# Kernel optimization log

Hardware: AMD Instinct MI355X
Metric: run time of the kernel (lower is better)

Reference implementation:

```python
import jax, jax.numpy as jnp
import numpy as np

B, S, D = 16, 4096, 64
SCALE = float(np.sqrt(D))  # sqrt(hidden_size)


def setup_inputs() -> dict:
    key = jax.random.key(0)
    kq, kk, kv = jax.random.split(key, 3)
    return {
        "query": jax.random.normal(kq, (B, S, D), dtype=jnp.float32),
        "key": jax.random.normal(kk, (B, S, D), dtype=jnp.float32),
        "value": jax.random.normal(kv, (B, S, D), dtype=jnp.float32),
    }


def reference(query, key, value):
    # energy: [B, S, S]
    energy = jnp.einsum("bqd,bkd->bqk", query, key) / SCALE
    attention = jax.nn.softmax(energy, axis=2)
    return jnp.einsum("bqk,bkd->bqd", attention, value)
```

## Files before the change

### kernel.cpp

```cpp
#include <hip/hip_runtime.h>


#define NBATCH 16
#define SEQ    4096
#define DIM    64
#define BQ     128
#define BK     64
#define NKT    (SEQ / BK)
#define NTILES (NBATCH * NKT)
#define TILEH  4096

#define QSCALE 0.180336879f

typedef _Float16 half2_t __attribute__((ext_vector_type(2)));
typedef _Float16 half4_t __attribute__((ext_vector_type(4)));
typedef _Float16 half8_t __attribute__((ext_vector_type(8)));
typedef float    floatx4 __attribute__((ext_vector_type(4)));

__device__ inline float fast_exp2(float x) {
#if __has_builtin(__builtin_amdgcn_exp2f)
  return __builtin_amdgcn_exp2f(x);
#else
  return exp2f(x);
#endif
}
__device__ inline float fast_rcp(float x) {
#if __has_builtin(__builtin_amdgcn_rcpf)
  return __builtin_amdgcn_rcpf(x);
#else
  return 1.0f / x;
#endif
}

__device__ inline int swz(int row, int col) {
  return row * 64 + ((((col >> 3) ^ ((row >> 1) & 7)) << 3) | (col & 7));
}

__device__ inline void async16(const void* g, void* l) {
  __builtin_amdgcn_global_load_lds(
      (const __attribute__((address_space(1))) void*)g,
      (__attribute__((address_space(3))) void*)l, 16, 0, 0);
}

__global__ __launch_bounds__(256, 2)
void prepack_kv(const float* __restrict__ Kg, const float* __restrict__ Vg,
                _Float16* __restrict__ Kh, _Float16* __restrict__ Vh)
{
  __shared__ __align__(16) _Float16 sVi[TILEH];
  const int tid = threadIdx.x;
  const int t16 = tid & 15;
  const int kg  = tid >> 4;
  const int bt  = blockIdx.x;
  const float* Kt_ = Kg + (size_t)bt * BK * DIM;
  const float* Vt_ = Vg + (size_t)bt * BK * DIM;

  floatx4 kbuf[4], vbuf[4];
  #pragma unroll
  for (int i = 0; i < 4; ++i) {
    const int key = kg + 16 * i;
    kbuf[i] = *(const floatx4*)(Kt_ + key * DIM + t16 * 4);
    vbuf[i] = *(const floatx4*)(Vt_ + key * DIM + t16 * 4);
  }
  {
    const int vbase = (kg >> 2) * 8 + (kg & 3) * 2;
    #pragma unroll
    for (int e = 0; e < 4; ++e) {
      const int dim = t16 * 4 + e;
      half2_t h0; h0[0] = (_Float16)vbuf[0][e]; h0[1] = (_Float16)vbuf[1][e];
      half2_t h1; h1[0] = (_Float16)vbuf[2][e]; h1[1] = (_Float16)vbuf[3][e];
      *(half2_t*)&sVi[swz(dim, vbase)]      = h0;
      *(half2_t*)&sVi[swz(dim, vbase + 32)] = h1;
    }
  }
  {
    _Float16* Ko = Kh + (size_t)bt * TILEH;
    #pragma unroll
    for (int i = 0; i < 4; ++i) {
      const int key = kg + 16 * i;
      half4_t h;
      #pragma unroll
      for (int j = 0; j < 4; ++j) h[j] = (_Float16)kbuf[i][j];
      *(half4_t*)&Ko[swz(key, t16 * 4)] = h;
    }
  }
  __syncthreads();
  half8_t* Vo = (half8_t*)(Vh + (size_t)bt * TILEH);
  const half8_t* Vs = (const half8_t*)sVi;
  Vo[tid] = Vs[tid]; Vo[tid + 256] = Vs[tid + 256];
}

__global__ __launch_bounds__(256, 2)
void attn_f16_flash(const float* __restrict__ Qg, const _Float16* __restrict__ Kh,
                    const _Float16* __restrict__ Vh, float* __restrict__ Og)
{
  __shared__ __align__(16) _Float16 sT[4][2 * TILEH];

  const int tid  = threadIdx.x;
  const int wave = tid >> 6;
  const int lane = tid & 63;
  const int l16  = lane & 15;
  const int quad = lane >> 4;
  const int hK   = (l16 >> 1) & 7;

  const int bid  = blockIdx.x;
  const int x    = bid & 7;
  const int r    = bid >> 3;
  const int b    = x + ((r & 1) << 3);
  const int qt   = r >> 1;
  const int q0   = qt * BQ + wave * 32;

  const float* Qb = Qg + ((size_t)b * SEQ + q0) * DIM;
  float*       Ob = Og + ((size_t)b * SEQ + q0) * DIM;

  half8_t qf[2][2];
  #pragma unroll
  for (int s = 0; s < 2; ++s)
    #pragma unroll
    for (int c = 0; c < 2; ++c) {
      const floatx4 f0 = *(const floatx4*)(Qb + (s * 16 + l16) * DIM + c * 32 + quad * 8);
      const floatx4 f1 = *(const floatx4*)(Qb + (s * 16 + l16) * DIM + c * 32 + quad * 8 + 4);
      half8_t h;
      #pragma unroll
      for (int j = 0; j < 4; ++j) h[j] = (_Float16)(f0[j] * QSCALE);
      #pragma unroll
      for (int j = 0; j < 4; ++j) h[4 + j] = (_Float16)(f1[j] * QSCALE);
      qf[s][c] = h;
    }

  half8_t vones;
  #pragma unroll
  for (int j = 0; j < 8; ++j) vones[j] = (_Float16)1.0f;

  floatx4 oacc2[4][2];
  floatx4 lacc[2];
  #pragma unroll
  for (int n = 0; n < 4; ++n)
    #pragma unroll
    for (int s = 0; s < 2; ++s) oacc2[n][s] = (floatx4){0.f, 0.f, 0.f, 0.f};
  #pragma unroll
  for (int s = 0; s < 2; ++s) lacc[s] = (floatx4){0.f, 0.f, 0.f, 0.f};

  #define ASYNC(KT, BUF)                                                       \
    do {                                                                       \
      const char* gk = (const char*)(Kh + ((size_t)b * NKT + (KT)) * TILEH)    \
                       + wave * 2048;                                          \
      const char* gv = (const char*)(Vh + ((size_t)b * NKT + (KT)) * TILEH)    \
                       + wave * 2048;                                          \
      char* lk = (char*)(&sT[BUF][0])     + wave * 2048;                       \
      char* lv = (char*)(&sT[BUF][TILEH]) + wave * 2048;                       \
      async16(gk + lane * 16,        lk);                                      \
      async16(gk + 1024 + lane * 16, lk + 1024);                               \
      async16(gv + lane * 16,        lv);                                      \
      async16(gv + 1024 + lane * 16, lv + 1024);                               \
    } while (0)

  #define QKH(scX, BUF, H)                                                     \
    do {                                                                       \
      const _Float16* SKB = &sT[BUF][0];                                       \
      _Pragma("unroll")                                                        \
      for (int k2 = 0; k2 < 2; ++k2)                                           \
        _Pragma("unroll")                                                      \
        for (int s = 0; s < 2; ++s) scX[k2][s] = (floatx4){0.f, 0.f, 0.f, 0.f};\
      _Pragma("unroll")                                                        \
      for (int k2 = 0; k2 < 2; ++k2) {                                         \
        const int nk = (H) * 2 + k2;                                           \
        _Pragma("unroll")                                                      \
        for (int c = 0; c < 2; ++c) {                                          \
          half8_t kf = *(const half8_t*)&SKB[(nk * 16 + l16) * 64 +            \
                                             (((c * 4 + quad) ^ hK) << 3)];    \
          _Pragma("unroll")                                                    \
          for (int s = 0; s < 2; ++s)                                          \
            scX[k2][s] = __builtin_amdgcn_mfma_f32_16x16x32_f16(               \
                kf, qf[s][c], scX[k2][s], 0, 0, 0);                            \
        }                                                                      \
      }                                                                        \
    } while (0)

  #define EXPH(scX, bfrX)                                                      \
    do {                                                                       \
      _Pragma("unroll")                                                        \
      for (int s = 0; s < 2; ++s) {                                            \
        half8_t bf;                                                            \
        _Pragma("unroll")                                                      \
        for (int j = 0; j < 8; ++j)                                            \
          bf[j] = (_Float16)fast_exp2(scX[j & 1][s][j >> 1]);                  \
        bfrX[s] = bf;                                                          \
      }                                                                        \
    } while (0)

  #define PVH(bfrX, BUF, H)                                                    \
    do {                                                                       \
      const _Float16* SVB = &sT[BUF][TILEH];                                   \
      _Pragma("unroll")                                                        \
      for (int n = 0; n < 4; ++n) {                                            \
        half8_t vf = *(const half8_t*)&SVB[(n * 16 + l16) * 64 +               \
                                           ((((H) * 4 + quad) ^ hK) << 3)];    \
        _Pragma("unroll")                                                      \
        for (int s = 0; s < 2; ++s)                                            \
          oacc2[n][s] = __builtin_amdgcn_mfma_f32_16x16x32_f16(                \
              vf, bfrX[s], oacc2[n][s], 0, 0, 0);                              \
      }                                                                        \
      _Pragma("unroll")                                                        \
      for (int s = 0; s < 2; ++s)                                              \
        lacc[s] = __builtin_amdgcn_mfma_f32_16x16x32_f16(                      \
            vones, bfrX[s], lacc[s], 0, 0, 0);                                 \
    } while (0)

  #define GATE(N)                                                              \
    do {                                                                       \
      asm volatile("s_waitcnt vmcnt(" #N ")" ::: "memory");                    \
      __builtin_amdgcn_s_barrier();                                            \
      __builtin_amdgcn_sched_barrier(0);                                       \
    } while (0)

  floatx4 scA[2][2], scB[2][2];
  half8_t bfrA[2], bfrB[2];

  #define STEP(TT, CB)                                                         \
    do {                                                                       \
      QKH(scB, CB, 1);                                \
      EXPH(scA, bfrA);                           \
      PVH(bfrA, CB, 0);                       \
      GATE(4);                                                                 \
      ASYNC((TT) + 3, ((CB) + 3) & 3);                                         \
      QKH(scA, ((CB) + 1) & 3, 0);           \
      EXPH(scB, bfrB);                                                         \
      PVH(bfrB, CB, 1);                      \
    } while (0)

  ASYNC(0, 0);
  ASYNC(1, 1);
  GATE(4);
  ASYNC(2, 2);
  QKH(scA, 0, 0);

  #pragma unroll 1
  for (int t = 0; t < NKT - 4; t += 4) {
    STEP(t + 0, 0);
    STEP(t + 1, 1);
    STEP(t + 2, 2);
    STEP(t + 3, 3);
  }
  STEP(60, 0);

  QKH(scB, 1, 1);
  EXPH(scA, bfrA);
  PVH(bfrA, 1, 0);
  GATE(4);
  QKH(scA, 2, 0);
  EXPH(scB, bfrB);
  PVH(bfrB, 1, 1);

  {
    QKH(scB, 2, 1);
    EXPH(scA, bfrA);
    PVH(bfrA, 2, 0);
    GATE(0);
    QKH(scA, 3, 0);
    EXPH(scB, bfrB);
    PVH(bfrB, 2, 1);
  }
  {
    QKH(scB, 3, 1);
    EXPH(scA, bfrA);
    PVH(bfrA, 3, 0);
    EXPH(scB, bfrB);
    PVH(bfrB, 3, 1);
  }

  #pragma unroll
  for (int s = 0; s < 2; ++s) {
    const float inv = fast_rcp(lacc[s][0]);
    #pragma unroll
    for (int n = 0; n < 4; ++n) {
      floatx4 o = oacc2[n][s];
      #pragma unroll
      for (int j = 0; j < 4; ++j) o[j] *= inv;
      *(floatx4*)&Ob[(s * 16 + l16) * DIM + n * 16 + quad * 4] = o;
    }
  }

  #undef ASYNC
  #undef QKH
  #undef EXPH
  #undef PVH
  #undef GATE
  #undef STEP
}

extern "C" void kernel_launch(void* const* d_in, const int* in_sizes, int n_in,
                              void* d_out, int out_size, void* d_ws, size_t ws_size,
                              hipStream_t stream) {
  const float* Q = (const float*)d_in[0];
  const float* K = (const float*)d_in[1];
  const float* V = (const float*)d_in[2];
  float* O  = (float*)d_out;
  (void)in_sizes; (void)n_in; (void)out_size; (void)ws_size;

  _Float16* Kh = (_Float16*)d_ws;
  _Float16* Vh = Kh + (size_t)NTILES * TILEH;

  prepack_kv<<<dim3(NTILES), dim3(256), 0, stream>>>(K, V, Kh, Vh);
  attn_f16_flash<<<dim3(NBATCH * (SEQ / BQ)), dim3(256), 0, stream>>>(
      Q, Kh, Vh, O);
}
```

Before: 156.4 us.

## Split each query tile across eight waves with sixteen rows per wave

The block grows from 256 to 512 threads and each wave now handles 16 query rows instead of 32. The per-wave Q fragments, score, exp and accumulator arrays shrink to one sub-tile, and the async K/V tile copy is spread over eight waves with one 16-byte load per lane each. Wait counts drop to match. This cuts register pressure and adds waves for latency hiding, but halves how many MFMAs reuse each LDS K/V fragment, so LDS read traffic per FLOP doubles.

```diff
diff --git a/kernel.cpp b/kernel.cpp
--- a/kernel.cpp
+++ b/kernel.cpp
@@ -89,7 +89,7 @@
   Vo[tid] = Vs[tid]; Vo[tid + 256] = Vs[tid + 256];
 }
 
-__global__ __launch_bounds__(256, 2)
+__global__ __launch_bounds__(512, 4)
 void attn_f16_flash(const float* __restrict__ Qg, const _Float16* __restrict__ Kh,
                     const _Float16* __restrict__ Vh, float* __restrict__ Og)
 {
@@ -107,60 +107,51 @@
   const int r    = bid >> 3;
   const int b    = x + ((r & 1) << 3);
   const int qt   = r >> 1;
-  const int q0   = qt * BQ + wave * 32;
+  const int q0   = qt * BQ + wave * 16;
 
   const float* Qb = Qg + ((size_t)b * SEQ + q0) * DIM;
   float*       Ob = Og + ((size_t)b * SEQ + q0) * DIM;
 
-  half8_t qf[2][2];
-  #pragma unroll
-  for (int s = 0; s < 2; ++s)
-    #pragma unroll
-    for (int c = 0; c < 2; ++c) {
-      const floatx4 f0 = *(const floatx4*)(Qb + (s * 16 + l16) * DIM + c * 32 + quad * 8);
-      const floatx4 f1 = *(const floatx4*)(Qb + (s * 16 + l16) * DIM + c * 32 + quad * 8 + 4);
-      half8_t h;
-      #pragma unroll
-      for (int j = 0; j < 4; ++j) h[j] = (_Float16)(f0[j] * QSCALE);
-      #pragma unroll
-      for (int j = 0; j < 4; ++j) h[4 + j] = (_Float16)(f1[j] * QSCALE);
-      qf[s][c] = h;
-    }
+  half8_t qf[2];
+  #pragma unroll
+  for (int c = 0; c < 2; ++c) {
+    const floatx4 f0 = *(const floatx4*)(Qb + l16 * DIM + c * 32 + quad * 8);
+    const floatx4 f1 = *(const floatx4*)(Qb + l16 * DIM + c * 32 + quad * 8 + 4);
+    half8_t h;
+    #pragma unroll
+    for (int j = 0; j < 4; ++j) h[j] = (_Float16)(f0[j] * QSCALE);
+    #pragma unroll
+    for (int j = 0; j < 4; ++j) h[4 + j] = (_Float16)(f1[j] * QSCALE);
+    qf[c] = h;
+  }
 
   half8_t vones;
   #pragma unroll
   for (int j = 0; j < 8; ++j) vones[j] = (_Float16)1.0f;
 
-  floatx4 oacc2[4][2];
-  floatx4 lacc[2];
-  #pragma unroll
-  for (int n = 0; n < 4; ++n)
-    #pragma unroll
-    for (int s = 0; s < 2; ++s) oacc2[n][s] = (floatx4){0.f, 0.f, 0.f, 0.f};
-  #pragma unroll
-  for (int s = 0; s < 2; ++s) lacc[s] = (floatx4){0.f, 0.f, 0.f, 0.f};
+  floatx4 oacc[4];
+  floatx4 lacc;
+  #pragma unroll
+  for (int n = 0; n < 4; ++n) oacc[n] = (floatx4){0.f, 0.f, 0.f, 0.f};
+  lacc = (floatx4){0.f, 0.f, 0.f, 0.f};
 
   #define ASYNC(KT, BUF)                                                       \
     do {                                                                       \
       const char* gk = (const char*)(Kh + ((size_t)b * NKT + (KT)) * TILEH)    \
-                       + wave * 2048;                                          \
+                       + wave * 1024;                                          \
       const char* gv = (const char*)(Vh + ((size_t)b * NKT + (KT)) * TILEH)    \
-                       + wave * 2048;                                          \
-      char* lk = (char*)(&sT[BUF][0])     + wave * 2048;                       \
-      char* lv = (char*)(&sT[BUF][TILEH]) + wave * 2048;                       \
-      async16(gk + lane * 16,        lk);                                      \
-      async16(gk + 1024 + lane * 16, lk + 1024);                               \
-      async16(gv + lane * 16,        lv);                                      \
-      async16(gv + 1024 + lane * 16, lv + 1024);                               \
+                       + wave * 1024;                                          \
+      char* lk = (char*)(&sT[BUF][0])     + wave * 1024;                       \
+      char* lv = (char*)(&sT[BUF][TILEH]) + wave * 1024;                       \
+      async16(gk + lane * 16, lk);                                             \
+      async16(gv + lane * 16, lv);                                             \
     } while (0)
 
   #define QKH(scX, BUF, H)                                                     \
     do {                                                                       \
       const _Float16* SKB = &sT[BUF][0];                                       \
       _Pragma("unroll")                                                        \
-      for (int k2 = 0; k2 < 2; ++k2)                                           \
-        _Pragma("unroll")                                                      \
-        for (int s = 0; s < 2; ++s) scX[k2][s] = (floatx4){0.f, 0.f, 0.f, 0.f};\
+      for (int k2 = 0; k2 < 2; ++k2) scX[k2] = (floatx4){0.f, 0.f, 0.f, 0.f};  \
       _Pragma("unroll")                                                        \
       for (int k2 = 0; k2 < 2; ++k2) {                                         \
         const int nk = (H) * 2 + k2;                                           \
@@ -168,24 +159,19 @@
         for (int c = 0; c < 2; ++c) {                                          \
           half8_t kf = *(const half8_t*)&SKB[(nk * 16 + l16) * 64 +            \
                                              (((c * 4 + quad) ^ hK) << 3)];    \
-          _Pragma("unroll")                                                    \
-          for (int s = 0; s < 2; ++s)                                          \
-            scX[k2][s] = __builtin_amdgcn_mfma_f32_16x16x32_f16(               \
-                kf, qf[s][c], scX[k2][s], 0, 0, 0);                            \
+          scX[k2] = __builtin_amdgcn_mfma_f32_16x16x32_f16(                    \
+              kf, qf[c], scX[k2], 0, 0, 0);                                    \
         }                                                                      \
       }                                                                        \
     } while (0)
 
   #define EXPH(scX, bfrX)                                                      \
     do {                                                                       \
-      _Pragma("unroll")                                                        \
-      for (int s = 0; s < 2; ++s) {                                            \
-        half8_t bf;                                                            \
-        _Pragma("unroll")                                                      \
-        for (int j = 0; j < 8; ++j)                                            \
-          bf[j] = (_Float16)fast_exp2(scX[j & 1][s][j >> 1]);                  \
-        bfrX[s] = bf;                                                          \
-      }                                                                        \
+      half8_t bf;                                                              \
+      _Pragma("unroll")                                                        \
+      for (int j = 0; j < 8; ++j)                                              \
+        bf[j] = (_Float16)fast_exp2(scX[j & 1][j >> 1]);                       \
+      bfrX = bf;                                                               \
     } while (0)
 
   #define PVH(bfrX, BUF, H)                                                    \
@@ -195,15 +181,11 @@
       for (int n = 0; n < 4; ++n) {                                            \
         half8_t vf = *(const half8_t*)&SVB[(n * 16 + l16) * 64 +               \
                                            ((((H) * 4 + quad) ^ hK) << 3)];    \
-        _Pragma("unroll")                                                      \
-        for (int s = 0; s < 2; ++s)                                            \
-          oacc2[n][s] = __builtin_amdgcn_mfma_f32_16x16x32_f16(                \
-              vf, bfrX[s], oacc2[n][s], 0, 0, 0);                              \
+        oacc[n] = __builtin_amdgcn_mfma_f32_16x16x32_f16(                      \
+            vf, bfrX, oacc[n], 0, 0, 0);                                       \
       }                                                                        \
-      _Pragma("unroll")                                                        \
-      for (int s = 0; s < 2; ++s)                                              \
-        lacc[s] = __builtin_amdgcn_mfma_f32_16x16x32_f16(                      \
-            vones, bfrX[s], lacc[s], 0, 0, 0);                                 \
+      lacc = __builtin_amdgcn_mfma_f32_16x16x32_f16(                           \
+          vones, bfrX, lacc, 0, 0, 0);                                         \
     } while (0)
 
   #define GATE(N)                                                              \
@@ -213,15 +195,15 @@
       __builtin_amdgcn_sched_barrier(0);                                       \
     } while (0)
 
-  floatx4 scA[2][2], scB[2][2];
-  half8_t bfrA[2], bfrB[2];
+  floatx4 scA[2], scB[2];
+  half8_t bfrA, bfrB;
 
   #define STEP(TT, CB)                                                         \
     do {                                                                       \
       QKH(scB, CB, 1);                                \
       EXPH(scA, bfrA);                           \
       PVH(bfrA, CB, 0);                       \
-      GATE(4);                                                                 \
+      GATE(2);                                                                 \
       ASYNC((TT) + 3, ((CB) + 3) & 3);                                         \
       QKH(scA, ((CB) + 1) & 3, 0);           \
       EXPH(scB, bfrB);                                                         \
@@ -230,7 +212,7 @@
 
   ASYNC(0, 0);
   ASYNC(1, 1);
-  GATE(4);
+  GATE(2);
   ASYNC(2, 2);
   QKH(scA, 0, 0);
 
@@ -246,7 +228,7 @@
   QKH(scB, 1, 1);
   EXPH(scA, bfrA);
   PVH(bfrA, 1, 0);
-  GATE(4);
+  GATE(2);
   QKH(scA, 2, 0);
   EXPH(scB, bfrB);
   PVH(bfrB, 1, 1);
@@ -268,15 +250,14 @@
     PVH(bfrB, 3, 1);
   }
 
-  #pragma unroll
-  for (int s = 0; s < 2; ++s) {
-    const float inv = fast_rcp(lacc[s][0]);
+  {
+    const float inv = fast_rcp(lacc[0]);
     #pragma unroll
     for (int n = 0; n < 4; ++n) {
-      floatx4 o = oacc2[n][s];
+      floatx4 o = oacc[n];
       #pragma unroll
       for (int j = 0; j < 4; ++j) o[j] *= inv;
-      *(floatx4*)&Ob[(s * 16 + l16) * DIM + n * 16 + quad * 4] = o;
+      *(floatx4*)&Ob[l16 * DIM + n * 16 + quad * 4] = o;
     }
   }
 
@@ -301,6 +282,6 @@
   _Float16* Vh = Kh + (size_t)NTILES * TILEH;
 
   prepack_kv<<<dim3(NTILES), dim3(256), 0, stream>>>(K, V, Kh, Vh);
-  attn_f16_flash<<<dim3(NBATCH * (SEQ / BQ)), dim3(256), 0, stream>>>(
+  attn_f16_flash<<<dim3(NBATCH * (SEQ / BQ)), dim3(512), 0, stream>>>(
       Q, Kh, Vh, O);
 }
```

Result: slower. 160.7 us (+2.7%).
